# Performance work log

Measured on AMD Instinct MI355X. Metric: run time of the kernel, lower is better.

Reference implementation:

```python
import jax, jax.numpy as jnp
import numpy as np

HEAD_NUM = 16
EMBED_DIM = 512


def setup_inputs() -> dict:
    key = jax.random.key(0)
    k1, k2, k3, k4, k5 = jax.random.split(key, 5)
    B, N, D = 8, 2048, EMBED_DIM
    x = jax.random.normal(k1, (B, N, D), dtype=jnp.float32)
    dis_matrix = jax.random.uniform(k2, (B, N, N), dtype=jnp.float32)
    s = 1.0 / np.sqrt(D)
    Wq = jax.random.normal(k3, (D, D), dtype=jnp.float32) * s
    Wk = jax.random.normal(k4, (D, D), dtype=jnp.float32) * s
    Wv = jax.random.normal(k5, (D, D), dtype=jnp.float32) * s
    alpha = jnp.float32(1.0)
    return {"x": x, "dis_matrix": dis_matrix, "Wq": Wq, "Wk": Wk, "Wv": Wv, "alpha": alpha}


def _split_heads(t, H):
    # [B, N, D] -> [B, H, N, D//H]
    B, N, D = t.shape
    return t.reshape(B, N, H, D // H).transpose(0, 2, 1, 3)


def reference(x, dis_matrix, Wq, Wk, Wv, alpha):
    B, N, D = x.shape
    H = HEAD_NUM
    # nn.Linear(bias=False): y = x @ W.T
    q = _split_heads(x @ Wq.T, H)  # [B,H,N,dk]
    k = _split_heads(x @ Wk.T, H)
    v = _split_heads(x @ Wv.T, H)
    log2n = jnp.float32(np.log2(N))
    dis_weight = jnp.exp(-alpha * log2n * dis_matrix)  # [B,N,N]
    k_weight = jnp.exp(k)
    # contract over source node i -> target node j
    weight_1 = jnp.einsum('bij,bhik->bhjk', dis_weight, k_weight * v)
    weight_2 = jnp.einsum('bij,bhik->bhjk', dis_weight, k_weight)
    out = jax.nn.sigmoid(q) * (weight_1 / weight_2)  # [B,H,N,dk]
    return out.transpose(0, 2, 1, 3).reshape(B, N, D)
```

## Files before the change

kernel.cpp:

```cpp
#include <hip/hip_runtime.h>
#include <math.h>
#include <stdint.h>


typedef __bf16 bf16_t;
typedef __attribute__((ext_vector_type(4))) __bf16 bf16x4;
typedef __attribute__((ext_vector_type(8))) __bf16 bf16x8;
typedef __attribute__((ext_vector_type(4))) float f32x4;

#define MFMA_BF16(a, b, c) __builtin_amdgcn_mfma_f32_16x16x32_bf16((a), (b), (c), 0, 0, 0)

static __device__ __forceinline__ void async_ld16(const bf16_t* g, bf16_t* lds) {
  __builtin_amdgcn_global_load_lds(
      reinterpret_cast<__attribute__((address_space(1))) unsigned int*>(
          reinterpret_cast<uintptr_t>(g)),
      reinterpret_cast<__attribute__((address_space(3))) unsigned int*>(
          reinterpret_cast<uintptr_t>(lds)),
      16, 0, 0);
}

template <int BK, int ROWS>
static __device__ __forceinline__ void stage(const bf16_t* g, int ldg, bf16_t* lds,
                                             int wv, int lane) {
  constexpr int CH = BK / 8;
  constexpr int RPW = 64 / CH;
  const int r_in = lane / CH;
  const int cpos = lane % CH;
#pragma unroll
  for (int s = 0; s < ROWS / (RPW * 4); ++s) {
    int rbase = wv * (ROWS / 4) + s * RPW;
    int row = rbase + r_in;
    int cg = cpos ^ ((row >> 1) & 3);
    async_ld16(g + (size_t)row * ldg + cg * 8, lds + rbase * BK + lane * 8);
  }
}

template <int BK>
static __device__ __forceinline__ bf16x8 frag_read(const bf16_t* lds, int row16,
                                                   int l15, int quad, int kc) {
  int p = (quad ^ ((l15 >> 1) & 3)) + kc * 4;
  return *(const bf16x8*)&lds[(row16 + l15) * BK + p * 8];
}

__global__ __launch_bounds__(256) void cvt_all(const float* __restrict__ x,
                                               const float* __restrict__ wq,
                                               const float* __restrict__ wk,
                                               const float* __restrict__ wv,
                                               bf16_t* __restrict__ xb,
                                               bf16_t* __restrict__ wall) {
  int i = blockIdx.x * 256 + threadIdx.x;
  if (i >= 2293760) return;
  const float* src;
  bf16_t* dst;
  int off;
  if (i < 2097152) {
    src = x; dst = xb; off = i;
  } else {
    int j = i - 2097152;
    int sel = j >> 16;
    off = j & 65535;
    src = (sel == 0) ? wq : (sel == 1) ? wk : wv;
    dst = wall + (size_t)sel * 262144;
  }
  f32x4 f = ((const f32x4*)src)[off];
  bf16x4 o;
  o[0] = (bf16_t)f[0]; o[1] = (bf16_t)f[1]; o[2] = (bf16_t)f[2]; o[3] = (bf16_t)f[3];
  ((bf16x4*)dst)[off] = o;
}

__global__ __launch_bounds__(256, 4) void proj_dw(const bf16_t* __restrict__ A,
                                                  const bf16_t* __restrict__ W,
                                                  bf16_t* __restrict__ qs,
                                                  bf16_t* __restrict__ kwT,
                                                  bf16_t* __restrict__ kwvT,
                                                  const float* __restrict__ dis,
                                                  bf16_t* __restrict__ dwT,
                                                  const float* __restrict__ alpha) {
  __shared__ __align__(16) char pool[32768];
  const int tid = threadIdx.x;
  const int idx = blockIdx.x;
  const int g19 = idx / 19, r19 = idx % 19;

  if (r19 >= 3) {
    int sub = g19 * 16 + (r19 - 3);
    int jt = sub & 31, it = (sub >> 5) & 31, b = sub >> 10;
    bf16_t* t = (bf16_t*)pool;
    const float coef = -alpha[0] * 11.0f;
    const int j0 = jt * 64, i0 = it * 64;
    const int rr = tid >> 4, cc = (tid & 15) * 4;
#pragma unroll
    for (int p = 0; p < 4; ++p) {
      int i = rr + p * 16;
      f32x4 d = *(const f32x4*)&dis[((size_t)(b * 2048 + i0 + i)) * 2048 + j0 + cc];
#pragma unroll
      for (int e = 0; e < 4; ++e) t[(cc + e) * 65 + i] = (bf16_t)__expf(coef * d[e]);
    }
    __syncthreads();
#pragma unroll
    for (int p = 0; p < 4; ++p) {
      int j = rr + p * 16;
      bf16x4 o;
#pragma unroll
      for (int e = 0; e < 4; ++e) o[e] = t[j * 65 + cc + e];
      *(bf16x4*)&dwT[((size_t)(b * 2048 + j0 + j)) * 2048 + i0 + cc] = o;
    }
    return;
  }

  const int sub = g19 * 3 + r19;
  const int m_blk = sub / 12, n_blk = sub % 12;
  bf16_t* As = (bf16_t*)pool;
  const int K = 512;
  const int wv = tid >> 6, lane = tid & 63;
  const int l15 = lane & 15, quad = lane >> 4;
  const int wm = wv >> 1, wn = wv & 1;
  const bf16_t* Am = A + (size_t)(m_blk * 128) * K;
  const int b = m_blk >> 4;

  if (n_blk < 4) {
    bf16_t* Bsq = (bf16_t*)(pool + 16384);
    const int c_loc = n_blk * 128;
    f32x4 acc[4][4];
#pragma unroll
    for (int a = 0; a < 4; ++a)
#pragma unroll
      for (int c = 0; c < 4; ++c) acc[a][c] = (f32x4){0.f, 0.f, 0.f, 0.f};

    for (int k0 = 0; k0 < K; k0 += 64) {
      stage<64, 128>(Am + k0, K, As, wv, lane);
      stage<64, 128>(W + (size_t)c_loc * K + k0, K, Bsq, wv, lane);
      __syncthreads();
#pragma unroll
      for (int kc = 0; kc < 2; ++kc) {
        bf16x8 a[4], bb[4];
#pragma unroll
        for (int mf = 0; mf < 4; ++mf) a[mf] = frag_read<64>(As, wm * 64 + mf * 16, l15, quad, kc);
#pragma unroll
        for (int nf = 0; nf < 4; ++nf) bb[nf] = frag_read<64>(Bsq, wn * 64 + nf * 16, l15, quad, kc);
#pragma unroll
        for (int mf = 0; mf < 4; ++mf)
#pragma unroll
          for (int nf = 0; nf < 4; ++nf) acc[mf][nf] = MFMA_BF16(a[mf], bb[nf], acc[mf][nf]);
      }
      __syncthreads();
    }
#pragma unroll
    for (int mf = 0; mf < 4; ++mf)
#pragma unroll
      for (int nf = 0; nf < 4; ++nf) {
        int j16 = (m_blk & 15) * 8 + wm * 4 + mf;
        int c16 = n_blk * 8 + wn * 4 + nf;
        bf16x4 o;
#pragma unroll
        for (int r = 0; r < 4; ++r)
          o[r] = (bf16_t)(1.0f / (1.0f + __expf(-acc[mf][nf][r])));
        size_t off = (((size_t)b * 128 + j16) * 32 + c16) * 256 + quad * 64 + l15 * 4;
        *(bf16x4*)&qs[off] = o;
      }
  } else {
    bf16_t* Bk = (bf16_t*)(pool + 16384);
    bf16_t* Bv = (bf16_t*)(pool + 24576);
    const int c_loc = (n_blk - 4) * 64;
    f32x4 acck[4][2], accv[4][2];
#pragma unroll
    for (int a = 0; a < 4; ++a)
#pragma unroll
      for (int c = 0; c < 2; ++c) {
        acck[a][c] = (f32x4){0.f, 0.f, 0.f, 0.f};
        accv[a][c] = (f32x4){0.f, 0.f, 0.f, 0.f};
      }
    const bf16_t* Wk = W + (size_t)(512 + c_loc) * K;
    const bf16_t* Wv = W + (size_t)(1024 + c_loc) * K;

    for (int k0 = 0; k0 < K; k0 += 64) {
      stage<64, 128>(Am + k0, K, As, wv, lane);
      stage<64, 64>(Wk + k0, K, Bk, wv, lane);
      stage<64, 64>(Wv + k0, K, Bv, wv, lane);
      __syncthreads();
#pragma unroll
      for (int kc = 0; kc < 2; ++kc) {
        bf16x8 a[4], bk[2], bv[2];
#pragma unroll
        for (int mf = 0; mf < 4; ++mf) a[mf] = frag_read<64>(As, wm * 64 + mf * 16, l15, quad, kc);
#pragma unroll
        for (int nf = 0; nf < 2; ++nf) {
          bk[nf] = frag_read<64>(Bk, wn * 32 + nf * 16, l15, quad, kc);
          bv[nf] = frag_read<64>(Bv, wn * 32 + nf * 16, l15, quad, kc);
        }
#pragma unroll
        for (int mf = 0; mf < 4; ++mf)
#pragma unroll
          for (int nf = 0; nf < 2; ++nf) {
            acck[mf][nf] = MFMA_BF16(a[mf], bk[nf], acck[mf][nf]);
            accv[mf][nf] = MFMA_BF16(a[mf], bv[nf], accv[mf][nf]);
          }
      }
      __syncthreads();
    }

    bf16_t* Lk = (bf16_t*)pool;
    bf16_t* Lv = (bf16_t*)(pool + 8704);
    const int t0 = (m_blk * 128) & 2047;
#pragma unroll
    for (int ci = 0; ci < 2; ++ci) {
      if (wn == ci) {
#pragma unroll
        for (int mf = 0; mf < 4; ++mf)
#pragma unroll
          for (int nf = 0; nf < 2; ++nf) {
            int cl = nf * 16 + l15;
            int tl = wm * 64 + mf * 16 + quad * 4;
#pragma unroll
            for (int r = 0; r < 4; ++r) {
              float kw = __expf(acck[mf][nf][r]);
              Lk[cl * 136 + tl + r] = (bf16_t)kw;
              Lv[cl * 136 + tl + r] = (bf16_t)(kw * accv[mf][nf][r]);
            }
          }
      }
      __syncthreads();
      {
        int rowt = tid >> 3, colt = (tid & 7) * 16;
        int c = c_loc + ci * 32 + rowt;
        size_t g = ((size_t)b * 512 + c) * 2048 + t0 + colt;
        *(bf16x8*)&kwT[g] = *(const bf16x8*)&Lk[rowt * 136 + colt];
        *(bf16x8*)&kwT[g + 8] = *(const bf16x8*)&Lk[rowt * 136 + colt + 8];
        *(bf16x8*)&kwvT[g] = *(const bf16x8*)&Lv[rowt * 136 + colt];
        *(bf16x8*)&kwvT[g + 8] = *(const bf16x8*)&Lv[rowt * 136 + colt + 8];
      }
      __syncthreads();
    }
  }
}

__global__ __launch_bounds__(256, 4) void main_gemm(const bf16_t* __restrict__ dwT,
                                                    const bf16_t* __restrict__ kwvT,
                                                    const bf16_t* __restrict__ kwT,
                                                    const bf16_t* __restrict__ qs,
                                                    float* __restrict__ out) {
  __shared__ bf16_t As[128 * 64];
  __shared__ bf16_t Bs[128 * 64];
  const int K = 2048;
  const int tid = threadIdx.x;
  const int wv = tid >> 6, lane = tid & 63;
  const int l15 = lane & 15, quad = lane >> 4;
  const int i = blockIdx.x;
  const int b = i & 7, nb = (i >> 3) & 7, mb = i >> 6;
  const int wm = wv >> 1, wn = wv & 1;

  const bf16_t* Ab = dwT + ((size_t)b * 2048 + mb * 128) * K;
  const bf16_t* Bv = kwvT + ((size_t)b * 512 + nb * 64) * K;
  const bf16_t* Bk = kwT + ((size_t)b * 512 + nb * 64) * K;
  const int r_in8 = lane >> 3, cpos8 = lane & 7;

  f32x4 acc[4][4];
#pragma unroll
  for (int a = 0; a < 4; ++a)
#pragma unroll
    for (int c = 0; c < 4; ++c) acc[a][c] = (f32x4){0.f, 0.f, 0.f, 0.f};

  for (int k0 = 0; k0 < K; k0 += 64) {
    stage<64, 128>(Ab + k0, K, As, wv, lane);
#pragma unroll
    for (int s = 0; s < 4; ++s) {
      int rbase = wv * 32 + s * 8;
      int row = rbase + r_in8;
      int type = (rbase >> 4) & 1;
      int c = ((rbase >> 5) << 4) + (row & 15);
      int cg = cpos8 ^ ((row >> 1) & 3);
      const bf16_t* src = type ? Bk : Bv;
      async_ld16(src + (size_t)c * K + k0 + cg * 8, Bs + rbase * 64 + lane * 8);
    }
    __syncthreads();
#pragma unroll
    for (int kc = 0; kc < 2; ++kc) {
      bf16x8 a[4], bb[4];
#pragma unroll
      for (int mf = 0; mf < 4; ++mf) a[mf] = frag_read<64>(As, wm * 64 + mf * 16, l15, quad, kc);
#pragma unroll
      for (int nf = 0; nf < 4; ++nf) bb[nf] = frag_read<64>(Bs, wn * 64 + nf * 16, l15, quad, kc);
#pragma unroll
      for (int mf = 0; mf < 4; ++mf)
#pragma unroll
        for (int nf = 0; nf < 4; ++nf) acc[mf][nf] = MFMA_BF16(a[mf], bb[nf], acc[mf][nf]);
    }
    __syncthreads();
  }

#pragma unroll
  for (int mf = 0; mf < 4; ++mf)
#pragma unroll
    for (int p = 0; p < 2; ++p) {
      f32x4 w1 = acc[mf][2 * p];
      f32x4 w2 = acc[mf][2 * p + 1];
      int j16 = mb * 8 + wm * 4 + mf;
      int c16 = nb * 4 + wn * 2 + p;
      size_t qoff = (((size_t)b * 128 + j16) * 32 + c16) * 256 + quad * 64 + l15 * 4;
      bf16x4 qv = *(const bf16x4*)&qs[qoff];
      int c = nb * 64 + (wn * 2 + p) * 16 + l15;
#pragma unroll
      for (int r = 0; r < 4; ++r) {
        int j = mb * 128 + wm * 64 + mf * 16 + quad * 4 + r;
        size_t idx = ((size_t)b * 2048 + j) * 512 + c;
        out[idx] = (float)qv[r] * (w1[r] / w2[r]);
      }
    }
}

extern "C" void kernel_launch(void* const* d_in, const int* in_sizes, int n_in,
                              void* d_out, int out_size, void* d_ws, size_t ws_size,
                              hipStream_t stream) {
  const float* x = (const float*)d_in[0];
  const float* dis = (const float*)d_in[1];
  const float* Wq = (const float*)d_in[2];
  const float* Wk = (const float*)d_in[3];
  const float* Wv = (const float*)d_in[4];
  const float* alpha = (const float*)d_in[5];
  float* out = (float*)d_out;

  char* p = (char*)d_ws;
  bf16_t* x_bf = (bf16_t*)p;  p += (size_t)16384 * 512 * 2;
  bf16_t* Wall = (bf16_t*)p;  p += (size_t)1536 * 512 * 2;
  bf16_t* kwT  = (bf16_t*)p;  p += (size_t)8 * 512 * 2048 * 2;
  bf16_t* kwvT = (bf16_t*)p;  p += (size_t)8 * 512 * 2048 * 2;
  bf16_t* dwT  = (bf16_t*)p;  p += (size_t)8 * 2048 * 2048 * 2;
  bf16_t* qs_bf = (bf16_t*)p; p += (size_t)16384 * 512 * 2;
  if ((size_t)(p - (char*)d_ws) > ws_size) return;

  cvt_all<<<8960, 256, 0, stream>>>(x, Wq, Wk, Wv, x_bf, Wall);
  proj_dw<<<9728, 256, 0, stream>>>(x_bf, Wall, qs_bf, kwT, kwvT, dis, dwT, alpha);
  main_gemm<<<1024, 256, 0, stream>>>(dwT, kwvT, kwT, qs_bf, out);
}
```

Measured before the change: 348.3 us.

## Restructure main GEMM into 256x256 tiles with double-buffered LDS and phased MFMA

Rewrites the main weighted-aggregation GEMM to use 512-thread blocks computing 256x256 output tiles, with double-buffered 128KB dynamic LDS so global->LDS loads for the next K-step overlap the MFMAs of the current one. Fragment loads and MFMA groups are interleaved in phases separated by barriers, with setprio raised around the MFMAs, and the LDS swizzle is changed to an XOR over 8 chunks. The larger tiles raise operand reuse per staged byte and drop the grid to 256 blocks. In exchange, occupancy falls to one block per CU because of the LDS footprint, and with 256 blocks the grid roughly matches the CU count, leaving little slack for load imbalance.

```diff
diff --git a/kernel.cpp b/kernel.cpp
--- a/kernel.cpp
+++ b/kernel.cpp
@@ -40,6 +40,12 @@
                                                    int l15, int quad, int kc) {
   int p = (quad ^ ((l15 >> 1) & 3)) + kc * 4;
   return *(const bf16x8*)&lds[(row16 + l15) * BK + p * 8];
+}
+
+static __device__ __forceinline__ bf16x8 frag3(const bf16_t* lds, int row16,
+                                               int l15, int quad, int kc) {
+  int p = (quad | (kc << 2)) ^ (l15 & 7);
+  return *(const bf16x8*)&lds[(row16 + l15) * 64 + p * 8];
 }
 
 __global__ __launch_bounds__(256) void cvt_all(const float* __restrict__ x,
@@ -233,76 +239,130 @@
   }
 }
 
-__global__ __launch_bounds__(256, 4) void main_gemm(const bf16_t* __restrict__ dwT,
+__global__ __launch_bounds__(512, 2) void main_gemm(const bf16_t* __restrict__ dwT,
                                                     const bf16_t* __restrict__ kwvT,
                                                     const bf16_t* __restrict__ kwT,
                                                     const bf16_t* __restrict__ qs,
                                                     float* __restrict__ out) {
-  __shared__ bf16_t As[128 * 64];
-  __shared__ bf16_t Bs[128 * 64];
+  extern __shared__ __align__(16) char smem_raw[];
+  bf16_t* const lds = (bf16_t*)smem_raw;
   const int K = 2048;
   const int tid = threadIdx.x;
   const int wv = tid >> 6, lane = tid & 63;
   const int l15 = lane & 15, quad = lane >> 4;
-  const int i = blockIdx.x;
-  const int b = i & 7, nb = (i >> 3) & 7, mb = i >> 6;
-  const int wm = wv >> 1, wn = wv & 1;
-
-  const bf16_t* Ab = dwT + ((size_t)b * 2048 + mb * 128) * K;
-  const bf16_t* Bv = kwvT + ((size_t)b * 512 + nb * 64) * K;
-  const bf16_t* Bk = kwT + ((size_t)b * 512 + nb * 64) * K;
-  const int r_in8 = lane >> 3, cpos8 = lane & 7;
-
-  f32x4 acc[4][4];
-#pragma unroll
-  for (int a = 0; a < 4; ++a)
-#pragma unroll
-    for (int c = 0; c < 4; ++c) acc[a][c] = (f32x4){0.f, 0.f, 0.f, 0.f};
-
-  for (int k0 = 0; k0 < K; k0 += 64) {
-    stage<64, 128>(Ab + k0, K, As, wv, lane);
-#pragma unroll
-    for (int s = 0; s < 4; ++s) {
-      int rbase = wv * 32 + s * 8;
-      int row = rbase + r_in8;
-      int type = (rbase >> 4) & 1;
-      int c = ((rbase >> 5) << 4) + (row & 15);
-      int cg = cpos8 ^ ((row >> 1) & 3);
-      const bf16_t* src = type ? Bk : Bv;
-      async_ld16(src + (size_t)c * K + k0 + cg * 8, Bs + rbase * 64 + lane * 8);
-    }
+  const int bi = blockIdx.x;
+  const int b = bi & 7, nbb = (bi >> 3) & 3, mb = bi >> 5;
+  const int wm = wv >> 2, wn = wv & 3;
+  const int r_in = lane >> 3, cpos = lane & 7;
+  const int cg = cpos ^ r_in;
+
+  const bf16_t* const Ab = dwT + ((size_t)b * 2048 + mb * 256) * K;
+  const bf16_t* const BvB = kwvT + (size_t)b * 512 * K;
+  const bf16_t* const BkB = kwT + (size_t)b * 512 * K;
+
+  const bf16_t* aSrc[4];
+  const bf16_t* bSrc[4];
+#pragma unroll
+  for (int s = 0; s < 4; ++s) {
+    const int row = s * 64 + wv * 8 + r_in;
+    aSrc[s] = Ab + (size_t)row * K + cg * 8;
+    const int type = (row >> 4) & 1;
+    const int crow = nbb * 128 + (row >> 5) * 16 + (row & 15);
+    const bf16_t* base = type ? BkB : BvB;
+    bSrc[s] = base + (size_t)crow * K + cg * 8;
+  }
+
+  f32x4 acc[8][4];
+#pragma unroll
+  for (int m = 0; m < 8; ++m)
+#pragma unroll
+    for (int n = 0; n < 4; ++n) acc[m][n] = (f32x4){0.f, 0.f, 0.f, 0.f};
+
+  bf16x8 a[8];
+  bf16x8 b0[4];
+  bf16x8 b1[4];
+
+#define STAGE_T(dst, koff)                                                         \
+  do {                                                                             \
+    bf16_t* A_ = lds + (dst)*32768;                                                \
+    _Pragma("unroll") for (int s = 0; s < 4; ++s)                                  \
+        async_ld16(aSrc[s] + (koff), A_ + s * 4096 + wv * 512 + lane * 8);         \
+    _Pragma("unroll") for (int s = 0; s < 4; ++s)                                  \
+        async_ld16(bSrc[s] + (koff), A_ + 16384 + s * 4096 + wv * 512 + lane * 8); \
+  } while (0)
+
+#define LOADA(As_, mh)                                                             \
+  do {                                                                             \
+    _Pragma("unroll") for (int mf = 0; mf < 4; ++mf)                               \
+        _Pragma("unroll") for (int kc = 0; kc < 2; ++kc)                           \
+            a[mf * 2 + kc] =                                                       \
+        frag3((As_), wm * 128 + (mh)*64 + mf * 16, l15, quad, kc);                 \
+  } while (0)
+
+#define LOADB(Bs_, dstarr, nh)                                                     \
+  do {                                                                             \
+    _Pragma("unroll") for (int nf = 0; nf < 2; ++nf)                               \
+        _Pragma("unroll") for (int kc = 0; kc < 2; ++kc)                           \
+            dstarr[nf * 2 + kc] =                                                  \
+        frag3((Bs_), wn * 64 + (nh)*32 + nf * 16, l15, quad, kc);                  \
+  } while (0)
+
+#define MFMA_PH(mh, nh, barr)                                                      \
+  do {                                                                             \
+    __builtin_amdgcn_s_setprio(1);                                                 \
+    _Pragma("unroll") for (int kc = 0; kc < 2; ++kc)                               \
+        _Pragma("unroll") for (int mf = 0; mf < 4; ++mf)                           \
+            _Pragma("unroll") for (int nf = 0; nf < 2; ++nf)                       \
+                acc[(mh)*4 + mf][(nh)*2 + nf] =                                    \
+        MFMA_BF16(a[mf * 2 + kc], barr[nf * 2 + kc], acc[(mh)*4 + mf][(nh)*2 + nf]); \
+    __builtin_amdgcn_s_setprio(0);                                                 \
+  } while (0)
+
+  STAGE_T(0, 0);
+  __syncthreads();
+
+  for (int t = 0; t < 32; ++t) {
+    const int c = t & 1;
+    const bf16_t* As_c = lds + c * 32768;
+    const bf16_t* Bs_c = As_c + 16384;
+    if (t < 31) STAGE_T(c ^ 1, (t + 1) * 64);
+    LOADA(As_c, 0);
+    LOADB(Bs_c, b0, 0);
+    __builtin_amdgcn_s_barrier();
+    MFMA_PH(0, 0, b0);
+    __builtin_amdgcn_s_barrier();
+    LOADB(Bs_c, b1, 1);
+    __builtin_amdgcn_s_barrier();
+    MFMA_PH(0, 1, b1);
+    __builtin_amdgcn_s_barrier();
+    LOADA(As_c, 1);
+    __builtin_amdgcn_s_barrier();
+    MFMA_PH(1, 1, b1);
+    __builtin_amdgcn_s_barrier();
+    MFMA_PH(1, 0, b0);
     __syncthreads();
-#pragma unroll
-    for (int kc = 0; kc < 2; ++kc) {
-      bf16x8 a[4], bb[4];
-#pragma unroll
-      for (int mf = 0; mf < 4; ++mf) a[mf] = frag_read<64>(As, wm * 64 + mf * 16, l15, quad, kc);
-#pragma unroll
-      for (int nf = 0; nf < 4; ++nf) bb[nf] = frag_read<64>(Bs, wn * 64 + nf * 16, l15, quad, kc);
-#pragma unroll
-      for (int mf = 0; mf < 4; ++mf)
-#pragma unroll
-        for (int nf = 0; nf < 4; ++nf) acc[mf][nf] = MFMA_BF16(a[mf], bb[nf], acc[mf][nf]);
-    }
-    __syncthreads();
-  }
-
-#pragma unroll
-  for (int mf = 0; mf < 4; ++mf)
+  }
+
+#undef STAGE_T
+#undef LOADA
+#undef LOADB
+#undef MFMA_PH
+
+#pragma unroll
+  for (int mf = 0; mf < 8; ++mf)
 #pragma unroll
     for (int p = 0; p < 2; ++p) {
       f32x4 w1 = acc[mf][2 * p];
       f32x4 w2 = acc[mf][2 * p + 1];
-      int j16 = mb * 8 + wm * 4 + mf;
-      int c16 = nb * 4 + wn * 2 + p;
+      const int j16 = mb * 16 + wm * 8 + mf;
+      const int c16 = nbb * 8 + wn * 2 + p;
       size_t qoff = (((size_t)b * 128 + j16) * 32 + c16) * 256 + quad * 64 + l15 * 4;
       bf16x4 qv = *(const bf16x4*)&qs[qoff];
-      int c = nb * 64 + (wn * 2 + p) * 16 + l15;
+      const int ccol = c16 * 16 + l15;
 #pragma unroll
       for (int r = 0; r < 4; ++r) {
-        int j = mb * 128 + wm * 64 + mf * 16 + quad * 4 + r;
-        size_t idx = ((size_t)b * 2048 + j) * 512 + c;
-        out[idx] = (float)qv[r] * (w1[r] / w2[r]);
+        const int j = j16 * 16 + quad * 4 + r;
+        out[((size_t)b * 2048 + j) * 512 + ccol] = (float)qv[r] * (w1[r] / w2[r]);
       }
     }
 }
@@ -327,7 +387,14 @@
   bf16_t* qs_bf = (bf16_t*)p; p += (size_t)16384 * 512 * 2;
   if ((size_t)(p - (char*)d_ws) > ws_size) return;
 
+  static bool attr_done = false;
+  if (!attr_done) {
+    hipFuncSetAttribute(reinterpret_cast<const void*>(main_gemm),
+                        hipFuncAttributeMaxDynamicSharedMemorySize, 131072);
+    attr_done = true;
+  }
+
   cvt_all<<<8960, 256, 0, stream>>>(x, Wq, Wk, Wv, x_bf, Wall);
   proj_dw<<<9728, 256, 0, stream>>>(x_bf, Wall, qs_bf, kwT, kwvT, dis, dwT, alpha);
-  main_gemm<<<1024, 256, 0, stream>>>(dwT, kwvT, kwT, qs_bf, out);
-}
+  main_gemm<<<256, 512, 131072, stream>>>(dwT, kwvT, kwT, qs_bf, out);
+}
```

After: 333.1 us. 4.4% less time.
